# Optimization experiments

Measured on AMD Instinct MI355X. Metric: run time of the kernel, lower is better.

Reference implementation:

```python
import jax, jax.numpy as jnp
import numpy as np

B, T, D_EMB, D_QKV = 8, 2048, 1024, 64
SCALE = 1.0 / (D_QKV ** 0.5)


def setup_inputs() -> dict:
    key = jax.random.key(0)
    kx, kq, kk, kv = jax.random.split(key, 4)
    return {
        "x": jax.random.normal(kx, (B, T, D_EMB), dtype=jnp.float32),
        "Wq": jax.random.normal(kq, (D_EMB, D_QKV), dtype=jnp.float32) * 0.02,
        "Wk": jax.random.normal(kk, (D_EMB, D_QKV), dtype=jnp.float32) * 0.02,
        "Wv": jax.random.normal(kv, (D_EMB, D_QKV), dtype=jnp.float32) * 0.02,
    }


def reference(x, Wq, Wk, Wv):
    # x: [B, T, D_emb]; projections to [B, T, D_qkv]
    q = jnp.einsum("bte,ed->btd", x, Wq)
    k = jnp.einsum("bte,ed->btd", x, Wk)
    v = jnp.einsum("bte,ed->btd", x, Wv)
    # scores: [B, T, T], scaled then causally masked
    scores = jnp.einsum("bqd,bkd->bqk", q, k) * SCALE
    t = x.shape[1]
    causal = jnp.tril(jnp.ones((t, t), dtype=bool))
    scores = jnp.where(causal[None, :, :], scores, -jnp.inf)
    attn = jax.nn.softmax(scores, axis=-1)
    return jnp.einsum("bqk,bkd->bqd", attn, v)
```

## Files before the change

kernel.cpp:

```cpp
#include <hip/hip_runtime.h>

typedef float f32x4 __attribute__((ext_vector_type(4)));
typedef __bf16 bf16x8 __attribute__((ext_vector_type(8)));
typedef __bf16 bf16x4 __attribute__((ext_vector_type(4)));

#define T_ 2048
#define DE 1024
#define DQ 64
#define SCALE 0.125f

#define GL16(gp, lp)                                                        \
  __builtin_amdgcn_global_load_lds(                                         \
      (const __attribute__((address_space(1))) void*)(gp),                  \
      (__attribute__((address_space(3))) void*)(lp), 16, 0, 0)

#define WAITVM(N) asm volatile("s_waitcnt vmcnt(" #N ")" ::: "memory")

__global__ __launch_bounds__(256) void kw_pack(
    const float* __restrict__ Wq, const float* __restrict__ Wk,
    const float* __restrict__ Wv, __bf16* __restrict__ Wf)
{
  int tid = blockIdx.x * 256 + threadIdx.x;
  int lane = tid & 63, f = tid >> 6;
  int t = f % 12, kc = f / 12;
  const float* W = (t < 4) ? Wq : ((t < 8) ? Wk : Wv);
  int nl = (t & 3) * 16 + (lane & 15);
  int k0 = kc * 32 + (lane >> 4) * 8;
  bf16x8 v;
#pragma unroll
  for (int j = 0; j < 8; ++j) v[j] = (__bf16)W[(size_t)(k0 + j) * 64 + nl];
  *(bf16x8*)(Wf + (size_t)tid * 8) = v;
}

__global__ __launch_bounds__(256) void kproj(
    const float* __restrict__ x, const __bf16* __restrict__ Wf,
    __bf16* __restrict__ Qb, __bf16* __restrict__ Kb, __bf16* __restrict__ Vt)
{
  __shared__ char lds[3 * 8192 + 2 * 24576];
  const int tid = threadIdx.x;
  const int lane = tid & 63;
  const int w = tid >> 6;
  const int col = lane & 15, g = lane >> 4;
  const int msub = w & 1;
  const int ng = w >> 1;
  const int mbase = blockIdx.x * 32;

  size_t gsrcA[2];
  int ldstA[2];
#pragma unroll
  for (int cc = 0; cc < 2; ++cc) {
    int q = w * 2 + cc;
    int row = q * 4 + (lane >> 4);
    int kbyte = ((lane & 15) * 16) ^ ((row & 7) << 4);
    gsrcA[cc] = (size_t)(mbase + row) * 4096 + (size_t)kbyte;
    ldstA[cc] = q * 1024 + lane * 16;
  }
  int ofsB[6];
#pragma unroll
  for (int cc = 0; cc < 6; ++cc) ofsB[cc] = (w * 6 + cc) * 1024 + lane * 16;

  f32x4 acc[6];
#pragma unroll
  for (int i = 0; i < 6; ++i) acc[i] = (f32x4){0.f, 0.f, 0.f, 0.f};

  const char* xb = (const char*)x;
  const char* wb = (const char*)Wf;

#define STAGE_A(ks)                                                         \
  {                                                                         \
    char* lb = &lds[((ks) % 3) * 8192];                                     \
    _Pragma("unroll")                                                       \
    for (int cc = 0; cc < 2; ++cc)                                          \
      GL16(xb + gsrcA[cc] + (size_t)(ks) * 256, lb + ldstA[cc]);            \
  }
#define STAGE_B(ks)                                                         \
  {                                                                         \
    char* lb = &lds[24576 + ((ks) & 1) * 24576];                            \
    _Pragma("unroll")                                                       \
    for (int cc = 0; cc < 6; ++cc)                                          \
      GL16(wb + (size_t)(ks) * 24576 + ofsB[cc], lb + ofsB[cc]);            \
  }
#define KSTEP(ks)                                                           \
  {                                                                         \
    const char* la = &lds[((ks) % 3) * 8192];                               \
    const char* lbB = &lds[24576 + ((ks) & 1) * 24576];                     \
    const int arow = msub * 16 + col;                                       \
    const char* abase = la + arow * 256;                                    \
    const int sw = (arow & 7) << 4;                                         \
    _Pragma("unroll")                                                       \
    for (int kh = 0; kh < 2; ++kh) {                                        \
      int kb = kh * 128 + g * 32;                                           \
      f32x4 a0 = *(const f32x4*)(abase + (kb ^ sw));                        \
      f32x4 a1 = *(const f32x4*)(abase + ((kb + 16) ^ sw));                 \
      bf16x8 af;                                                            \
      _Pragma("unroll")                                                     \
      for (int j = 0; j < 4; ++j) { af[j] = (__bf16)a0[j]; af[4 + j] = (__bf16)a1[j]; } \
      _Pragma("unroll")                                                     \
      for (int ii = 0; ii < 6; ++ii) {                                      \
        int nt = ng * 6 + ii;                                               \
        bf16x8 bfr = *(const bf16x8*)(lbB + ((kh * 12 + nt) * 64 + lane) * 16); \
        acc[ii] = __builtin_amdgcn_mfma_f32_16x16x32_bf16(af, bfr, acc[ii], 0, 0, 0); \
      }                                                                     \
    }                                                                       \
  }
#define ITER(ks, vm, doB, doA)                                              \
  WAITVM(vm);                                                               \
  __builtin_amdgcn_s_barrier();                                             \
  __builtin_amdgcn_sched_barrier(0);                                        \
  if (doB) STAGE_B((ks) + 1);                                               \
  if (doA) STAGE_A((ks) + 2);                                               \
  KSTEP(ks);

  STAGE_A(0);
  STAGE_B(0);
  STAGE_A(1);

  ITER(0, 2, 1, 1)  ITER(1, 2, 1, 1)  ITER(2, 2, 1, 1)  ITER(3, 2, 1, 1)
  ITER(4, 2, 1, 1)  ITER(5, 2, 1, 1)  ITER(6, 2, 1, 1)  ITER(7, 2, 1, 1)
  ITER(8, 2, 1, 1)  ITER(9, 2, 1, 1)  ITER(10, 2, 1, 1) ITER(11, 2, 1, 1)
  ITER(12, 2, 1, 1) ITER(13, 2, 1, 1) ITER(14, 2, 1, 0) ITER(15, 0, 0, 0)

#undef ITER
#undef KSTEP
#undef STAGE_B
#undef STAGE_A

  const int b = mbase >> 11;
  const int mrow = mbase + msub * 16 + g * 4;
  const int trow = (mbase & 2047) + msub * 16 + g * 4;
#pragma unroll
  for (int ii = 0; ii < 6; ++ii) {
    int ti = ng * 6 + ii;
    if (ti < 8) {
      __bf16* dst = (ti < 4) ? Qb : Kb;
      int c = (ti & 3) * 16 + col;
#pragma unroll
      for (int r = 0; r < 4; ++r)
        dst[(size_t)(mrow + r) * DQ + c] = (__bf16)acc[ii][r];
    } else {
      int d = (ti - 8) * 16 + col;
      bf16x4 v;
#pragma unroll
      for (int r = 0; r < 4; ++r) v[r] = (__bf16)acc[ii][r];
      *(bf16x4*)(Vt + ((size_t)(b * DQ + d)) * T_ + trow) = v;
    }
  }
}

__global__ __launch_bounds__(256) void kattn(
    const __bf16* __restrict__ Qb, const __bf16* __restrict__ Kb,
    const __bf16* __restrict__ Vt, float* __restrict__ out)
{
  __shared__ float accs[4][32][68];
  __shared__ float mls[4][2][32];
  __shared__ __bf16 plds[4][2][16][72];

  const int tid = threadIdx.x;
  const int lane = tid & 63;
  const int w = tid >> 6;
  const int col = lane & 15, g = lane >> 4;
  const int b = blockIdx.x & 7;
  const int jq = 63 - (blockIdx.x >> 3);
  const int qbase = jq * 32;

  bf16x8 qa[2][2];
#pragma unroll
  for (int mt = 0; mt < 2; ++mt) {
    const __bf16* Qp = Qb + (size_t)(b * T_ + qbase + mt * 16 + col) * DQ + g * 8;
    qa[mt][0] = *(const bf16x8*)(Qp);
    qa[mt][1] = *(const bf16x8*)(Qp + 32);
  }

  const __bf16* Kbb = Kb + (size_t)b * T_ * DQ;
  const __bf16* Vbb = Vt + (size_t)b * DQ * T_;

  f32x4 acc[2][4];
#pragma unroll
  for (int mt = 0; mt < 2; ++mt)
#pragma unroll
    for (int dt = 0; dt < 4; ++dt) acc[mt][dt] = (f32x4){0.f,0.f,0.f,0.f};
  float mrun[2][4], lsum[2][4];
#pragma unroll
  for (int mt = 0; mt < 2; ++mt)
#pragma unroll
    for (int r = 0; r < 4; ++r) { mrun[mt][r] = -1e30f; lsum[mt][r] = 0.f; }

  const int nb = (jq >> 1) + 1;
  for (int it = w; it < nb; it += 4) {
    const int nbase = it * 64;

    bf16x8 kf_[4][2];
#pragma unroll
    for (int nt = 0; nt < 4; ++nt) {
      const __bf16* Kp = Kbb + (size_t)(nbase + nt * 16 + col) * DQ + g * 8;
      kf_[nt][0] = *(const bf16x8*)(Kp);
      kf_[nt][1] = *(const bf16x8*)(Kp + 32);
    }

    f32x4 s[2][4];
#pragma unroll
    for (int mt = 0; mt < 2; ++mt)
#pragma unroll
      for (int nt = 0; nt < 4; ++nt) {
        f32x4 t = __builtin_amdgcn_mfma_f32_16x16x32_bf16(qa[mt][0], kf_[nt][0],
                                                          (f32x4){0.f,0.f,0.f,0.f}, 0, 0, 0);
        s[mt][nt] = __builtin_amdgcn_mfma_f32_16x16x32_bf16(qa[mt][1], kf_[nt][1], t, 0, 0, 0);
      }

    bf16x8 vf[4][2];
#pragma unroll
    for (int dt = 0; dt < 4; ++dt) {
      const __bf16* Vp = Vbb + (size_t)(dt * 16 + col) * T_ + nbase + g * 8;
      vf[dt][0] = *(const bf16x8*)(Vp);
      vf[dt][1] = *(const bf16x8*)(Vp + 32);
    }

#pragma unroll
    for (int mt = 0; mt < 2; ++mt)
#pragma unroll
      for (int nt = 0; nt < 4; ++nt)
#pragma unroll
        for (int r = 0; r < 4; ++r) s[mt][nt][r] *= SCALE;
    if (it == nb - 1) {
#pragma unroll
      for (int mt = 0; mt < 2; ++mt)
#pragma unroll
        for (int nt = 0; nt < 4; ++nt)
#pragma unroll
          for (int r = 0; r < 4; ++r)
            if (nbase + nt * 16 + col > qbase + mt * 16 + g * 4 + r) s[mt][nt][r] = -1e30f;
    }

    float mv[2][4];
#pragma unroll
    for (int mt = 0; mt < 2; ++mt)
#pragma unroll
      for (int r = 0; r < 4; ++r)
        mv[mt][r] = fmaxf(fmaxf(s[mt][0][r], s[mt][1][r]), fmaxf(s[mt][2][r], s[mt][3][r]));
#pragma unroll
    for (int sh = 1; sh <= 8; sh <<= 1)
#pragma unroll
      for (int mt = 0; mt < 2; ++mt)
#pragma unroll
        for (int r = 0; r < 4; ++r) mv[mt][r] = fmaxf(mv[mt][r], __shfl_xor(mv[mt][r], sh, 64));

#pragma unroll
    for (int mt = 0; mt < 2; ++mt)
#pragma unroll
      for (int r = 0; r < 4; ++r) {
        float mn = fmaxf(mrun[mt][r], mv[mt][r]);
        float rs = __expf(mrun[mt][r] - mn);
        mrun[mt][r] = mn;
        float ps = 0.f;
#pragma unroll
        for (int nt = 0; nt < 4; ++nt) {
          s[mt][nt][r] = __expf(s[mt][nt][r] - mn);
          ps += s[mt][nt][r];
        }
        lsum[mt][r] = lsum[mt][r] * rs + ps;
#pragma unroll
        for (int dt = 0; dt < 4; ++dt) acc[mt][dt][r] *= rs;
      }

#pragma unroll
    for (int mt = 0; mt < 2; ++mt)
#pragma unroll
      for (int nt = 0; nt < 4; ++nt)
#pragma unroll
        for (int r = 0; r < 4; ++r)
          plds[w][mt][g * 4 + r][nt * 16 + col] = (__bf16)s[mt][nt][r];

    bf16x8 pa[2][2];
#pragma unroll
    for (int mt = 0; mt < 2; ++mt) {
      pa[mt][0] = *(const bf16x8*)&plds[w][mt][col][g * 8];
      pa[mt][1] = *(const bf16x8*)&plds[w][mt][col][32 + g * 8];
    }

#pragma unroll
    for (int mt = 0; mt < 2; ++mt)
#pragma unroll
      for (int dt = 0; dt < 4; ++dt) {
        f32x4 t = __builtin_amdgcn_mfma_f32_16x16x32_bf16(pa[mt][0], vf[dt][0], acc[mt][dt], 0, 0, 0);
        acc[mt][dt] = __builtin_amdgcn_mfma_f32_16x16x32_bf16(pa[mt][1], vf[dt][1], t, 0, 0, 0);
      }
  }

#pragma unroll
  for (int sh = 1; sh <= 8; sh <<= 1)
#pragma unroll
    for (int mt = 0; mt < 2; ++mt)
#pragma unroll
      for (int r = 0; r < 4; ++r) lsum[mt][r] += __shfl_xor(lsum[mt][r], sh, 64);

#pragma unroll
  for (int mt = 0; mt < 2; ++mt)
#pragma unroll
    for (int r = 0; r < 4; ++r) {
      int row = mt * 16 + g * 4 + r;
      accs[w][row][col]      = acc[mt][0][r];
      accs[w][row][col + 16] = acc[mt][1][r];
      accs[w][row][col + 32] = acc[mt][2][r];
      accs[w][row][col + 48] = acc[mt][3][r];
      if (col == 0) { mls[w][0][row] = mrun[mt][r]; mls[w][1][row] = lsum[mt][r]; }
    }
  __syncthreads();

#pragma unroll
  for (int pass = 0; pass < 2; ++pass) {
    int row = pass * 16 + (tid >> 4);
    int c4 = (tid & 15) * 4;
    float m0 = mls[0][0][row], m1 = mls[1][0][row];
    float m2 = mls[2][0][row], m3 = mls[3][0][row];
    float M = fmaxf(fmaxf(m0, m1), fmaxf(m2, m3));
    float s0 = __expf(m0 - M), s1 = __expf(m1 - M);
    float s2 = __expf(m2 - M), s3 = __expf(m3 - M);
    float L = s0 * mls[0][1][row] + s1 * mls[1][1][row]
            + s2 * mls[2][1][row] + s3 * mls[3][1][row];
    f32x4 a0 = *(const f32x4*)&accs[0][row][c4];
    f32x4 a1 = *(const f32x4*)&accs[1][row][c4];
    f32x4 a2 = *(const f32x4*)&accs[2][row][c4];
    f32x4 a3 = *(const f32x4*)&accs[3][row][c4];
    float inv = 1.f / L;
    f32x4 o;
#pragma unroll
    for (int j = 0; j < 4; ++j)
      o[j] = (s0 * a0[j] + s1 * a1[j] + s2 * a2[j] + s3 * a3[j]) * inv;
    *(f32x4*)(out + (size_t)(b * T_ + qbase + row) * DQ + c4) = o;
  }
}

extern "C" void kernel_launch(void* const* d_in, const int* in_sizes, int n_in,
                              void* d_out, int out_size, void* d_ws, size_t ws_size,
                              hipStream_t stream)
{
  const float* x  = (const float*)d_in[0];
  const float* Wq = (const float*)d_in[1];
  const float* Wk = (const float*)d_in[2];
  const float* Wv = (const float*)d_in[3];
  float* out = (float*)d_out;

  char* ws = (char*)d_ws;
  __bf16* Wf = (__bf16*)(ws);
  __bf16* Qb = (__bf16*)(ws + 0x80000);
  __bf16* Kb = (__bf16*)(ws + 0x80000 + 0x200000);
  __bf16* Vt = (__bf16*)(ws + 0x80000 + 0x400000);

  kw_pack<<<96, 256, 0, stream>>>(Wq, Wk, Wv, Wf);
  kproj<<<512, 256, 0, stream>>>(x, Wf, Qb, Kb, Vt);
  kattn<<<512, 256, 0, stream>>>(Qb, Kb, Vt, out);
}
```

Before: 50.94 us.

## Load projection weights into registers, add lazy softmax rescale and MFMA priority

The projection kernel stops staging the packed weight matrix through LDS. Each wave now loads its weight fragments from global memory straight into double-buffered registers, which shrinks LDS use and removes LDS reads in the inner loop, at the cost of more VGPRs. The attention kernel skips the running-max shuffle reduction and the accumulator rescale unless some row's new max exceeds the stored max by more than a threshold of 8. It also raises wave priority around the MFMA blocks. The lazy rescale relies on fp32 headroom to stay correct, and the extra register arrays may lower occupancy.

After: 53.26 us. 4.5% more time.

```diff
diff --git a/kernel.cpp b/kernel.cpp
--- a/kernel.cpp
+++ b/kernel.cpp
@@ -36,13 +36,13 @@
     const float* __restrict__ x, const __bf16* __restrict__ Wf,
     __bf16* __restrict__ Qb, __bf16* __restrict__ Kb, __bf16* __restrict__ Vt)
 {
-  __shared__ char lds[3 * 8192 + 2 * 24576];
+  __shared__ float xs[3][32 * 64];
   const int tid = threadIdx.x;
   const int lane = tid & 63;
   const int w = tid >> 6;
   const int col = lane & 15, g = lane >> 4;
   const int msub = w & 1;
-  const int ng = w >> 1;
+  const int ng6 = (w >> 1) * 6;
   const int mbase = blockIdx.x * 32;
 
   size_t gsrcA[2];
@@ -55,9 +55,6 @@
     gsrcA[cc] = (size_t)(mbase + row) * 4096 + (size_t)kbyte;
     ldstA[cc] = q * 1024 + lane * 16;
   }
-  int ofsB[6];
-#pragma unroll
-  for (int cc = 0; cc < 6; ++cc) ofsB[cc] = (w * 6 + cc) * 1024 + lane * 16;
 
   f32x4 acc[6];
 #pragma unroll
@@ -65,28 +62,30 @@
 
   const char* xb = (const char*)x;
   const char* wb = (const char*)Wf;
+  const int arow = msub * 16 + col;
+  const int sw = (arow & 7) << 4;
+
+  bf16x8 bX[2][6], bY[2][6];
 
 #define STAGE_A(ks)                                                         \
   {                                                                         \
-    char* lb = &lds[((ks) % 3) * 8192];                                     \
+    char* lb = (char*)&xs[(ks) % 3][0];                                     \
     _Pragma("unroll")                                                       \
     for (int cc = 0; cc < 2; ++cc)                                          \
       GL16(xb + gsrcA[cc] + (size_t)(ks) * 256, lb + ldstA[cc]);            \
   }
-#define STAGE_B(ks)                                                         \
+#define LOADB(ks, B)                                                        \
   {                                                                         \
-    char* lb = &lds[24576 + ((ks) & 1) * 24576];                            \
     _Pragma("unroll")                                                       \
-    for (int cc = 0; cc < 6; ++cc)                                          \
-      GL16(wb + (size_t)(ks) * 24576 + ofsB[cc], lb + ofsB[cc]);            \
-  }
-#define KSTEP(ks)                                                           \
+    for (int kh = 0; kh < 2; ++kh)                                          \
+      _Pragma("unroll")                                                     \
+      for (int ii = 0; ii < 6; ++ii)                                        \
+        B[kh][ii] = *(const bf16x8*)(wb +                                   \
+            ((size_t)(((ks) * 2 + kh) * 12 + ng6 + ii) * 64 + lane) * 16);  \
+  }
+#define KSTEP(ks, B)                                                        \
   {                                                                         \
-    const char* la = &lds[((ks) % 3) * 8192];                               \
-    const char* lbB = &lds[24576 + ((ks) & 1) * 24576];                     \
-    const int arow = msub * 16 + col;                                       \
-    const char* abase = la + arow * 256;                                    \
-    const int sw = (arow & 7) << 4;                                         \
+    const char* abase = (const char*)&xs[(ks) % 3][0] + arow * 256;         \
     _Pragma("unroll")                                                       \
     for (int kh = 0; kh < 2; ++kh) {                                        \
       int kb = kh * 128 + g * 32;                                           \
@@ -96,33 +95,36 @@
       _Pragma("unroll")                                                     \
       for (int j = 0; j < 4; ++j) { af[j] = (__bf16)a0[j]; af[4 + j] = (__bf16)a1[j]; } \
       _Pragma("unroll")                                                     \
-      for (int ii = 0; ii < 6; ++ii) {                                      \
-        int nt = ng * 6 + ii;                                               \
-        bf16x8 bfr = *(const bf16x8*)(lbB + ((kh * 12 + nt) * 64 + lane) * 16); \
-        acc[ii] = __builtin_amdgcn_mfma_f32_16x16x32_bf16(af, bfr, acc[ii], 0, 0, 0); \
-      }                                                                     \
+      for (int ii = 0; ii < 6; ++ii)                                        \
+        acc[ii] = __builtin_amdgcn_mfma_f32_16x16x32_bf16(af, B[kh][ii], acc[ii], 0, 0, 0); \
     }                                                                       \
   }
-#define ITER(ks, vm, doB, doA)                                              \
+#define ITER(ks, vm, doB, doA, BLOAD, BUSE)                                 \
   WAITVM(vm);                                                               \
   __builtin_amdgcn_s_barrier();                                             \
   __builtin_amdgcn_sched_barrier(0);                                        \
-  if (doB) STAGE_B((ks) + 1);                                               \
+  if (doB) LOADB((ks) + 1, BLOAD);                                          \
+  __builtin_amdgcn_sched_barrier(0);                                        \
   if (doA) STAGE_A((ks) + 2);                                               \
-  KSTEP(ks);
+  __builtin_amdgcn_sched_barrier(0);                                        \
+  KSTEP(ks, BUSE);
 
   STAGE_A(0);
-  STAGE_B(0);
+  LOADB(0, bX);
   STAGE_A(1);
 
-  ITER(0, 2, 1, 1)  ITER(1, 2, 1, 1)  ITER(2, 2, 1, 1)  ITER(3, 2, 1, 1)
-  ITER(4, 2, 1, 1)  ITER(5, 2, 1, 1)  ITER(6, 2, 1, 1)  ITER(7, 2, 1, 1)
-  ITER(8, 2, 1, 1)  ITER(9, 2, 1, 1)  ITER(10, 2, 1, 1) ITER(11, 2, 1, 1)
-  ITER(12, 2, 1, 1) ITER(13, 2, 1, 1) ITER(14, 2, 1, 0) ITER(15, 0, 0, 0)
+  ITER(0, 2, 1, 1, bY, bX)   ITER(1, 2, 1, 1, bX, bY)
+  ITER(2, 2, 1, 1, bY, bX)   ITER(3, 2, 1, 1, bX, bY)
+  ITER(4, 2, 1, 1, bY, bX)   ITER(5, 2, 1, 1, bX, bY)
+  ITER(6, 2, 1, 1, bY, bX)   ITER(7, 2, 1, 1, bX, bY)
+  ITER(8, 2, 1, 1, bY, bX)   ITER(9, 2, 1, 1, bX, bY)
+  ITER(10, 2, 1, 1, bY, bX)  ITER(11, 2, 1, 1, bX, bY)
+  ITER(12, 2, 1, 1, bY, bX)  ITER(13, 2, 1, 1, bX, bY)
+  ITER(14, 2, 1, 0, bY, bX)  ITER(15, 0, 0, 0, bX, bY)
 
 #undef ITER
 #undef KSTEP
-#undef STAGE_B
+#undef LOADB
 #undef STAGE_A
 
   const int b = mbase >> 11;
@@ -130,7 +132,7 @@
   const int trow = (mbase & 2047) + msub * 16 + g * 4;
 #pragma unroll
   for (int ii = 0; ii < 6; ++ii) {
-    int ti = ng * 6 + ii;
+    int ti = ng6 + ii;
     if (ti < 8) {
       __bf16* dst = (ti < 4) ? Qb : Kb;
       int c = (ti & 3) * 16 + col;
@@ -198,6 +200,7 @@
     }
 
     f32x4 s[2][4];
+    __builtin_amdgcn_s_setprio(1);
 #pragma unroll
     for (int mt = 0; mt < 2; ++mt)
 #pragma unroll
@@ -206,6 +209,7 @@
                                                           (f32x4){0.f,0.f,0.f,0.f}, 0, 0, 0);
         s[mt][nt] = __builtin_amdgcn_mfma_f32_16x16x32_bf16(qa[mt][1], kf_[nt][1], t, 0, 0, 0);
       }
+    __builtin_amdgcn_s_setprio(0);
 
     bf16x8 vf[4][2];
 #pragma unroll
@@ -231,36 +235,62 @@
             if (nbase + nt * 16 + col > qbase + mt * 16 + g * 4 + r) s[mt][nt][r] = -1e30f;
     }
 
-    float mv[2][4];
+    float pmax[2][4];
 #pragma unroll
     for (int mt = 0; mt < 2; ++mt)
 #pragma unroll
       for (int r = 0; r < 4; ++r)
-        mv[mt][r] = fmaxf(fmaxf(s[mt][0][r], s[mt][1][r]), fmaxf(s[mt][2][r], s[mt][3][r]));
-#pragma unroll
-    for (int sh = 1; sh <= 8; sh <<= 1)
+        pmax[mt][r] = fmaxf(fmaxf(s[mt][0][r], s[mt][1][r]), fmaxf(s[mt][2][r], s[mt][3][r]));
+    bool need = false;
+#pragma unroll
+    for (int mt = 0; mt < 2; ++mt)
+#pragma unroll
+      for (int r = 0; r < 4; ++r)
+        need = need || (pmax[mt][r] > mrun[mt][r] + 8.f);
+
+    if (__any(need)) {
+      float mv[2][4];
 #pragma unroll
       for (int mt = 0; mt < 2; ++mt)
 #pragma unroll
-        for (int r = 0; r < 4; ++r) mv[mt][r] = fmaxf(mv[mt][r], __shfl_xor(mv[mt][r], sh, 64));
-
-#pragma unroll
-    for (int mt = 0; mt < 2; ++mt)
-#pragma unroll
-      for (int r = 0; r < 4; ++r) {
-        float mn = fmaxf(mrun[mt][r], mv[mt][r]);
-        float rs = __expf(mrun[mt][r] - mn);
-        mrun[mt][r] = mn;
-        float ps = 0.f;
-#pragma unroll
-        for (int nt = 0; nt < 4; ++nt) {
-          s[mt][nt][r] = __expf(s[mt][nt][r] - mn);
-          ps += s[mt][nt][r];
+        for (int r = 0; r < 4; ++r) mv[mt][r] = pmax[mt][r];
+#pragma unroll
+      for (int sh = 1; sh <= 8; sh <<= 1)
+#pragma unroll
+        for (int mt = 0; mt < 2; ++mt)
+#pragma unroll
+          for (int r = 0; r < 4; ++r) mv[mt][r] = fmaxf(mv[mt][r], __shfl_xor(mv[mt][r], sh, 64));
+#pragma unroll
+      for (int mt = 0; mt < 2; ++mt)
+#pragma unroll
+        for (int r = 0; r < 4; ++r) {
+          float mn = fmaxf(mrun[mt][r], mv[mt][r]);
+          float rs = __expf(mrun[mt][r] - mn);
+          mrun[mt][r] = mn;
+          float ps = 0.f;
+#pragma unroll
+          for (int nt = 0; nt < 4; ++nt) {
+            s[mt][nt][r] = __expf(s[mt][nt][r] - mn);
+            ps += s[mt][nt][r];
+          }
+          lsum[mt][r] = lsum[mt][r] * rs + ps;
+#pragma unroll
+          for (int dt = 0; dt < 4; ++dt) acc[mt][dt][r] *= rs;
         }
-        lsum[mt][r] = lsum[mt][r] * rs + ps;
-#pragma unroll
-        for (int dt = 0; dt < 4; ++dt) acc[mt][dt][r] *= rs;
-      }
+    } else {
+#pragma unroll
+      for (int mt = 0; mt < 2; ++mt)
+#pragma unroll
+        for (int r = 0; r < 4; ++r) {
+          float ps = 0.f;
+#pragma unroll
+          for (int nt = 0; nt < 4; ++nt) {
+            s[mt][nt][r] = __expf(s[mt][nt][r] - mrun[mt][r]);
+            ps += s[mt][nt][r];
+          }
+          lsum[mt][r] += ps;
+        }
+    }
 
 #pragma unroll
     for (int mt = 0; mt < 2; ++mt)
@@ -277,6 +307,7 @@
       pa[mt][1] = *(const bf16x8*)&plds[w][mt][col][32 + g * 8];
     }
 
+    __builtin_amdgcn_s_setprio(1);
 #pragma unroll
     for (int mt = 0; mt < 2; ++mt)
 #pragma unroll
@@ -284,6 +315,7 @@
         f32x4 t = __builtin_amdgcn_mfma_f32_16x16x32_bf16(pa[mt][0], vf[dt][0], acc[mt][dt], 0, 0, 0);
         acc[mt][dt] = __builtin_amdgcn_mfma_f32_16x16x32_bf16(pa[mt][1], vf[dt][1], t, 0, 0, 0);
       }
+    __builtin_amdgcn_s_setprio(0);
   }
 
 #pragma unroll
```
